# Performance work log

Measured on AMD Instinct MI355X. Metric: run time of the kernel, lower is better.

The kernel has to match this reference:

```python
import jax, jax.numpy as jnp
import numpy as np
from jax import lax

RADIUS = 0.1
K_LOCAL = 32
N_CENTROIDS = 2048


def farthest_point_sample(pos, m):
    # Greedy FPS, deterministic start at index 0 (torch version uses a random start).
    pos = lax.stop_gradient(pos)  # index selection is non-differentiable
    N = pos.shape[0]
    big = jnp.finfo(pos.dtype).max

    def step(carry, _):
        dist, current = carry
        d2 = jnp.sum((pos - pos[current]) ** 2, axis=-1)  # (N,)
        dist = jnp.minimum(dist, d2)
        nxt = jnp.argmax(dist).astype(jnp.int32)
        return (dist, nxt), current

    init = (jnp.full((N,), big, dtype=pos.dtype), jnp.int32(0))
    _, idx = lax.scan(step, init, None, length=m)
    return idx  # (m,) int32


def ball_query(pos, centers, radius, k):
    # (M, N) pairwise squared distances -- same dense form as the torch reference.
    d2 = jnp.sum((centers[:, None, :] - pos[None, :, :]) ** 2, axis=-1)
    within = d2 <= radius * radius
    big = jnp.finfo(d2.dtype).max
    masked = jnp.where(within, d2, big)
    _, idx = lax.top_k(-masked, k)              # k smallest distances
    valid = jnp.take_along_axis(within, idx, axis=1)
    fallback = jnp.broadcast_to(idx[:, :1], idx.shape)
    return jnp.where(valid, idx, fallback)      # (M, k) padded with first (nearest) idx


def setup_inputs() -> dict:
    key = jax.random.key(0)
    ks = jax.random.split(key, 5)
    N, C = 50000, 128
    scale = 1.0 / np.sqrt(C)
    return {
        "pos": jax.random.uniform(ks[0], (N, 3), dtype=jnp.float32),
        "feat_scalar": jax.random.normal(ks[1], (N, C, 1), dtype=jnp.float32),
        "feat_vector": jax.random.normal(ks[2], (N, C, 3), dtype=jnp.float32),
        "W_scalar": jax.random.normal(ks[3], (C, C), dtype=jnp.float32) * scale,
        "W_vector": jax.random.normal(ks[4], (C, C), dtype=jnp.float32) * scale,
        "b_scalar": jnp.zeros((C,), dtype=jnp.float32),
        "b_vector": jnp.zeros((C,), dtype=jnp.float32),
    }


def reference(pos, feat_scalar, feat_vector, W_scalar, W_vector, b_scalar, b_vector):
    M = min(N_CENTROIDS, pos.shape[0])
    cent_idx = farthest_point_sample(pos, M)          # (M,)
    centroids = pos[cent_idx]                         # (M, 3)
    nbr_idx = ball_query(pos, centroids, RADIUS, K_LOCAL)  # (M, k)

    def pool_mix(f, W, b):
        f_nbr = f[nbr_idx]                            # (M, k, C, d) gather
        f_pooled = jnp.max(f_nbr, axis=1)             # (M, C, d) max-pool over neighbors
        # ChannelMixer: linear mix across channel dim
        return jnp.einsum('mcd,co->mod', f_pooled, W) + b[None, :, None]

    out_scalar = pool_mix(feat_scalar, W_scalar, b_scalar)
    out_vector = pool_mix(feat_vector, W_vector, b_vector)
    return centroids, out_scalar, out_vector
```

## Files before the change

### kernel.cpp

```cpp
#include <hip/hip_runtime.h>
#include <float.h>

#define N_PTS   50000
#define M_CENT  2048
#define K_LOC   32
#define C_CH    128

typedef unsigned long long u64;
typedef unsigned int u32;

#define FPS_NB    14
#define FPS_GRID  128
#define FPS_NT    512
#define FPS_PPT   7
#define FPS_R     64
#define SLOT_U64  8
#define ROW_U64   (FPS_NB*SLOT_U64)
#define FPS_FAST_TRIPS 256
#define FPS_POLL_BOUND (1<<16)

__global__ void init_ws_kernel(u64* __restrict__ slots) {
  int t = blockIdx.x * blockDim.x + threadIdx.x;
  if (t < FPS_R * FPS_NB * SLOT_U64) slots[t] = 0ull;
}

__device__ __forceinline__ void fast_store(u64* p, u64 v) {
  asm volatile("global_store_dwordx2 %0, %1, off sc0"
               :: "v"(p), "v"(v) : "memory");
}
__device__ __forceinline__ u64 fresh_load(const u64* p) {
  u64 v;
  asm volatile("buffer_inv sc0\n\t"
               "global_load_dwordx2 %0, %1, off\n\t"
               "s_waitcnt vmcnt(0)"
               : "=v"(v) : "v"(p) : "memory");
  return v;
}
__device__ __forceinline__ u64 sc1_load(const u64* p) {
  return __hip_atomic_load(p, __ATOMIC_RELAXED, __HIP_MEMORY_SCOPE_AGENT);
}
template <bool SAFE>
__device__ __forceinline__ void slot_store(u64* p, u64 v) {
  if (SAFE) __hip_atomic_store(p, v, __ATOMIC_RELAXED, __HIP_MEMORY_SCOPE_AGENT);
  else      fast_store(p, v);
}

template <int CTRL>
__device__ __forceinline__ u32 dppmov_u(u32 v) {
  return (u32)__builtin_amdgcn_update_dpp((int)v, (int)v, CTRL, 0xf, 0xf, false);
}
template <int CTRL>
__device__ __forceinline__ float dppmov_f(float v) {
  return __int_as_float(
      __builtin_amdgcn_update_dpp(__float_as_int(v), __float_as_int(v),
                                  CTRL, 0xf, 0xf, false));
}
__device__ __forceinline__ float wave_max_f32(float v) {
  v = fmaxf(v, dppmov_f<0x111>(v));
  v = fmaxf(v, dppmov_f<0x112>(v));
  v = fmaxf(v, dppmov_f<0x114>(v));
  v = fmaxf(v, dppmov_f<0x118>(v));
  v = fmaxf(v, dppmov_f<0x142>(v));
  v = fmaxf(v, dppmov_f<0x143>(v));
  return __int_as_float(__builtin_amdgcn_readlane(__float_as_int(v), 63));
}
__device__ __forceinline__ u32 wave_max_u32(u32 v) {
  u32 t;
  t = dppmov_u<0x111>(v); v = v > t ? v : t;
  t = dppmov_u<0x112>(v); v = v > t ? v : t;
  t = dppmov_u<0x114>(v); v = v > t ? v : t;
  t = dppmov_u<0x118>(v); v = v > t ? v : t;
  t = dppmov_u<0x142>(v); v = v > t ? v : t;
  t = dppmov_u<0x143>(v); v = v > t ? v : t;
  return (u32)__builtin_amdgcn_readlane((int)v, 63);
}
__device__ __forceinline__ u32 wave_min_u32(u32 v) {
  u32 t;
  t = dppmov_u<0x111>(v); v = v < t ? v : t;
  t = dppmov_u<0x112>(v); v = v < t ? v : t;
  t = dppmov_u<0x114>(v); v = v < t ? v : t;
  t = dppmov_u<0x118>(v); v = v < t ? v : t;
  t = dppmov_u<0x142>(v); v = v < t ? v : t;
  t = dppmov_u<0x143>(v); v = v < t ? v : t;
  return (u32)__builtin_amdgcn_readlane((int)v, 63);
}

template <bool SAFE>
__device__ __forceinline__ void fps_main(
    const float* __restrict__ pos, u64* __restrict__ slots,
    float* __restrict__ cent_out, const int wid,
    uint2 (*s_w)[FPS_NT/64], float (*s_bc)[3])
{
  const int lane = threadIdx.x & 63;
  const int wv   = threadIdx.x >> 6;
  const int w    = wid * (FPS_NT/64) + wv;

  float px[FPS_PPT], py[FPS_PPT], pz[FPS_PPT], dist[FPS_PPT];
#pragma unroll
  for (int j = 0; j < FPS_PPT; j++) {
    int n = (w * FPS_PPT + j) * 64 + lane;
    if (n < N_PTS) {
      px[j] = pos[3*n+0]; py[j] = pos[3*n+1]; pz[j] = pos[3*n+2];
      dist[j] = FLT_MAX;
    } else {
      px[j] = 0.f; py[j] = 0.f; pz[j] = 0.f; dist[j] = -1.f;
    }
  }

  bool broken   = false;
  bool distrust = false;

  float cx = pos[0], cy = pos[1], cz = pos[2];

  for (int i = 0; i < M_CENT; i++) {
    if (wid == 0 && wv == 0 && lane == 0) {
      cent_out[3*i+0] = cx; cent_out[3*i+1] = cy; cent_out[3*i+2] = cz;
    }
    float lmax = -1.0f;
#pragma unroll
    for (int j = 0; j < FPS_PPT; j++) {
      int n = (w * FPS_PPT + j) * 64 + lane;
      if (n < N_PTS) {
        float dx = __fsub_rn(px[j], cx);
        float dy = __fsub_rn(py[j], cy);
        float dz = __fsub_rn(pz[j], cz);
        float d2 = __fadd_rn(__fadd_rn(__fmul_rn(dx,dx), __fmul_rn(dy,dy)),
                             __fmul_rn(dz,dz));
        float d  = fminf(dist[j], d2);
        dist[j] = d;
        lmax = fmaxf(lmax, d);
      }
    }
    float wmax = wave_max_f32(lmax);
    u32 li = 0xFFFFFFFFu;
#pragma unroll
    for (int j = 0; j < FPS_PPT; j++) {
      int n = (w * FPS_PPT + j) * 64 + lane;
      if (n < N_PTS && dist[j] == wmax) li = li < (u32)n ? li : (u32)n;
    }
    u32 widx = wave_min_u32(li);

    if (i == M_CENT - 1) break;

    if (lane == 0) s_w[i & 1][wv] = make_uint2(__float_as_uint(wmax), widx);
    __syncthreads();

    if (wv == 0) {
      uint2 kv = (lane < FPS_NT/64) ? s_w[i & 1][lane]
                                    : make_uint2(0u, 0xFFFFFFFFu);
      u32 bmaxb = wave_max_u32(kv.x);
      u32 bidx  = wave_min_u32(kv.x == bmaxb ? kv.y : 0xFFFFFFFFu);
      u64 ownkey = ((u64)bmaxb << 32) | (u64)(0xFFFFFFFFu - bidx);
      u64* row = slots + (size_t)(i & (FPS_R-1)) * ROW_U64;

      u64 got;
      if (!SAFE && broken) {
        got = (lane == wid) ? ownkey : 1ull;
      } else {
        if (lane == 0) {
          slot_store<SAFE>(&row[wid * SLOT_U64], ownkey);
          if (i >= 2)
            slot_store<SAFE>(&slots[(size_t)((i-2) & (FPS_R-1)) * ROW_U64
                                    + wid * SLOT_U64], 0ull);
        }
        got = (lane < FPS_NB) ? 0ull : 1ull;
        u64* sl = row + lane * SLOT_U64;
        if (!SAFE) {
          if (!distrust) {
            int t = 0;
            while (__ballot(got == 0ull) && t < FPS_FAST_TRIPS) {
              if (got == 0ull) got = fresh_load(sl);
              ++t;
            }
            if (__ballot(got == 0ull)) distrust = true;
          }
          int trips = 0;
          while (__ballot(got == 0ull)) {
            if (got == 0ull) got = sc1_load(sl);
            if (++trips > FPS_POLL_BOUND) {
              if (got == 0ull) got = 1ull;
              broken = true;
            }
          }
        } else {
          while (__ballot(got == 0ull)) {
            if (got == 0ull) got = sc1_load(sl);
          }
        }
      }
      u32 hi = (u32)(got >> 32), lo = (u32)got;
      u32 ic = 0xFFFFFFFFu - lo;
      if (ic >= N_PTS) ic = 0;
      float qx = 0.f, qy = 0.f, qz = 0.f;
      if (lane < FPS_NB) { qx = pos[3*ic]; qy = pos[3*ic+1]; qz = pos[3*ic+2]; }

      u32 H  = wave_max_u32(lane < FPS_NB ? hi : 0u);
      u32 LO = wave_max_u32((lane < FPS_NB && hi == H) ? lo : 0u);
      u64 msk = __ballot(lane < FPS_NB && hi == H && lo == LO);
      int L = __ffsll((long long)msk) - 1;
      float ncx = __int_as_float(__builtin_amdgcn_readlane(__float_as_int(qx), L));
      float ncy = __int_as_float(__builtin_amdgcn_readlane(__float_as_int(qy), L));
      float ncz = __int_as_float(__builtin_amdgcn_readlane(__float_as_int(qz), L));
      if (lane == 0) {
        s_bc[i & 1][0] = ncx; s_bc[i & 1][1] = ncy; s_bc[i & 1][2] = ncz;
      }
    }
    __syncthreads();
    cx = s_bc[i & 1][0]; cy = s_bc[i & 1][1]; cz = s_bc[i & 1][2];
  }
}

__global__ __launch_bounds__(FPS_NT) void fps_kernel(
    const float* __restrict__ pos,
    u64* __restrict__ slots,
    float* __restrict__ cent_out)
{
  __shared__ uint2 s_w[2][FPS_NT/64];
  __shared__ float s_bc[2][3];
  __shared__ int   s_role[2];

  if (threadIdx.x == 0) {
    u32 xcc;
    asm volatile("s_getreg_b32 %0, hwreg(HW_REG_XCC_ID, 0, 4)" : "=s"(xcc));
    xcc &= 7u;
    u64* cntp = slots + 63*ROW_U64 + (size_t)xcc * SLOT_U64 + 1;
    u64* winp = slots + 63*ROW_U64 + 8 * SLOT_U64 + 1;
    u64 t = __hip_atomic_fetch_add(cntp, 1ull, __ATOMIC_RELAXED,
                                   __HIP_MEMORY_SCOPE_AGENT);
    int ticket = (int)t;
    if (ticket == FPS_NB - 1) {
      u64 exp = 0ull;
      __hip_atomic_compare_exchange_strong(winp, &exp, (u64)(xcc + 1),
          __ATOMIC_RELAXED, __ATOMIC_RELAXED, __HIP_MEMORY_SCOPE_AGENT);
    }
    int role = -1, safe = 0;
    if (ticket < FPS_NB) {
      u64 win;
      do {
        win = __hip_atomic_load(winp, __ATOMIC_RELAXED, __HIP_MEMORY_SCOPE_AGENT);
        if (win == 0ull) __builtin_amdgcn_s_sleep(1);
      } while (win == 0ull);
      if (win == (u64)(xcc + 1)) {
        role = ticket;
        u64* hs = slots + 61*ROW_U64;
        bool okk = true;
        for (int r = 1; r <= 3 && okk; ++r) {
          fast_store(hs + (size_t)role * SLOT_U64 + 1, (u64)r);
          bool seen_all = false;
          for (int trip = 0; trip < 128 && !seen_all; ++trip) {
            int seen = 0;
            for (int j = 0; j < FPS_NB; ++j)
              seen += (fresh_load(hs + (size_t)j * SLOT_U64 + 1) >= (u64)r);
            seen_all = (seen == FPS_NB);
            if (!seen_all) __builtin_amdgcn_s_sleep(4);
          }
          okk = seen_all;
        }
        u64* okp = slots + 62*ROW_U64;
        __hip_atomic_store(okp + (size_t)role * SLOT_U64 + 1,
                           okk ? 2ull : 1ull,
                           __ATOMIC_RELAXED, __HIP_MEMORY_SCOPE_AGENT);
        for (int j = 0; j < FPS_NB; ++j) {
          u64 v;
          do {
            v = __hip_atomic_load(okp + (size_t)j * SLOT_U64 + 1,
                                  __ATOMIC_RELAXED, __HIP_MEMORY_SCOPE_AGENT);
            if (v == 0ull) __builtin_amdgcn_s_sleep(1);
          } while (v == 0ull);
          if (v == 1ull) safe = 1;
        }
      }
    }
    s_role[0] = role; s_role[1] = safe;
  }
  __syncthreads();
  const int wid = s_role[0];
  if (wid < 0) return;
  if (s_role[1]) fps_main<true >(pos, slots, cent_out, wid, s_w, s_bc);
  else           fps_main<false>(pos, slots, cent_out, wid, s_w, s_bc);
}

#define BQ_NT  256
#define BQ_CAP 2048

__global__ __launch_bounds__(BQ_NT) void ballq_kernel(
    const float* __restrict__ pos,
    const float* __restrict__ cent,
    int* __restrict__ nbr,
    int* __restrict__ nsel)
{
  __shared__ float s_d2[BQ_CAP];
  __shared__ int   s_idx[BQ_CAP];
  __shared__ int   s_count;
  __shared__ u64   s_red[BQ_NT/64];
  __shared__ u64   s_win;

  const int m = blockIdx.x, tid = threadIdx.x;
  if (tid == 0) s_count = 0;
  __syncthreads();
  const float cx = cent[3*m+0], cy = cent[3*m+1], cz = cent[3*m+2];

  for (int n = tid; n < N_PTS; n += BQ_NT) {
    float dx = __fsub_rn(cx, pos[3*n+0]);
    float dy = __fsub_rn(cy, pos[3*n+1]);
    float dz = __fsub_rn(cz, pos[3*n+2]);
    float d2 = __fadd_rn(__fadd_rn(__fmul_rn(dx,dx), __fmul_rn(dy,dy)),
                         __fmul_rn(dz,dz));
    if (d2 <= 0.01f) {
      int p = atomicAdd(&s_count, 1);
      if (p < BQ_CAP) { s_d2[p] = d2; s_idx[p] = n; }
    }
  }
  __syncthreads();
  int cnt = s_count; if (cnt > BQ_CAP) cnt = BQ_CAP;
  int ns = cnt < K_LOC ? cnt : K_LOC;

  for (int sel = 0; sel < ns; sel++) {
    u64 best = ~0ull;
    for (int p = tid; p < cnt; p += BQ_NT) {
      u64 pk = ((u64)__float_as_uint(s_d2[p]) << 32) | (u64)(u32)s_idx[p];
      if (pk < best) best = pk;
    }
#pragma unroll
    for (int off = 32; off >= 1; off >>= 1) {
      u64 o = __shfl_down(best, off, 64);
      if (o < best) best = o;
    }
    if ((tid & 63) == 0) s_red[tid >> 6] = best;
    __syncthreads();
    if (tid < 64) {
      best = (tid < BQ_NT/64) ? s_red[tid] : ~0ull;
#pragma unroll
      for (int off = 2; off >= 1; off >>= 1) {
        u64 o = __shfl_down(best, off, 64);
        if (o < best) best = o;
      }
      if (tid == 0) s_win = best;
    }
    __syncthreads();
    int widx = (int)(u32)(s_win & 0xFFFFFFFFull);
    if (tid == 0) nbr[m*K_LOC + sel] = widx;
    for (int p = tid; p < cnt; p += BQ_NT) {
      if (s_idx[p] == widx) s_d2[p] = FLT_MAX;
    }
    __syncthreads();
  }
  if (tid == 0) nsel[m] = ns;
}

__global__ __launch_bounds__(C_CH) void pool_mix_kernel(
    const float* __restrict__ fs,
    const float* __restrict__ fv,
    const float* __restrict__ Ws,
    const float* __restrict__ Wv,
    const float* __restrict__ bs,
    const float* __restrict__ bv,
    const int* __restrict__ nbr,
    const int* __restrict__ nsel,
    float* __restrict__ out_s,
    float* __restrict__ out_v)
{
  __shared__ float ps[C_CH];
  __shared__ float pv[C_CH*3];
  const int m = blockIdx.x, o = threadIdx.x;
  const int ns = nsel[m];
  float mS = -FLT_MAX, m0 = -FLT_MAX, m1 = -FLT_MAX, m2 = -FLT_MAX;
  for (int j = 0; j < ns; j++) {
    int n = nbr[m*K_LOC + j];
    mS = fmaxf(mS, fs[(size_t)n*C_CH + o]);
    const float* r = fv + (size_t)n*(C_CH*3) + 3*o;
    m0 = fmaxf(m0, r[0]); m1 = fmaxf(m1, r[1]); m2 = fmaxf(m2, r[2]);
  }
  ps[o] = mS; pv[3*o+0] = m0; pv[3*o+1] = m1; pv[3*o+2] = m2;
  __syncthreads();
  float aS = bs[o];
  float a0 = bv[o], a1 = bv[o], a2 = bv[o];
  for (int cc = 0; cc < C_CH; cc++) {
    float w1 = Ws[cc*C_CH + o];
    float w2 = Wv[cc*C_CH + o];
    aS = fmaf(ps[cc], w1, aS);
    a0 = fmaf(pv[3*cc+0], w2, a0);
    a1 = fmaf(pv[3*cc+1], w2, a1);
    a2 = fmaf(pv[3*cc+2], w2, a2);
  }
  out_s[(size_t)m*C_CH + o] = aS;
  float* ov = out_v + (size_t)m*(C_CH*3) + 3*o;
  ov[0] = a0; ov[1] = a1; ov[2] = a2;
}

extern "C" void kernel_launch(void* const* d_in, const int* in_sizes, int n_in,
                              void* d_out, int out_size, void* d_ws, size_t ws_size,
                              hipStream_t stream) {
  (void)in_sizes; (void)n_in; (void)out_size; (void)ws_size;
  const float* pos = (const float*)d_in[0];
  const float* fs  = (const float*)d_in[1];
  const float* fv  = (const float*)d_in[2];
  const float* Ws  = (const float*)d_in[3];
  const float* Wv  = (const float*)d_in[4];
  const float* bs  = (const float*)d_in[5];
  const float* bv  = (const float*)d_in[6];

  float* out      = (float*)d_out;
  float* cent_out = out;
  float* out_s    = out + 3*M_CENT;
  float* out_v    = out + 3*M_CENT + M_CENT*C_CH;

  char* ws = (char*)d_ws;
  u64* slots = (u64*)ws;
  size_t slots_bytes = (size_t)FPS_R * FPS_NB * SLOT_U64 * 8;
  int* nbr   = (int*)(ws + slots_bytes);
  int* nsel  = (int*)(ws + slots_bytes + (size_t)M_CENT*K_LOC*4);

  init_ws_kernel<<<(FPS_R*FPS_NB*SLOT_U64 + 255)/256, 256, 0, stream>>>(slots);
  fps_kernel<<<FPS_GRID, FPS_NT, 0, stream>>>(pos, slots, cent_out);
  ballq_kernel<<<M_CENT, BQ_NT, 0, stream>>>(pos, cent_out, nbr, nsel);
  pool_mix_kernel<<<M_CENT, C_CH, 0, stream>>>(fs, fv, Ws, Wv, bs, bv,
                                               nbr, nsel, out_s, out_v);
}
```

Measured before the change: 3.663 ms.

## Launch oversized FPS grid and elect one block per distinct CU per XCC

The FPS launch grows from 128 to 1024 blocks. Each block claims its hardware CU id (from HW_ID) through a CAS table, and only the first block to land on a given CU in an XCC gets a ticket. The first XCC with 14 distinct-CU blocks becomes the worker set, with a fallback election after all blocks arrive or a timeout. The aim is for the 14 cooperating FPS blocks to sit on separate CUs of one XCC, which should cut contention and speed up the spin-barrier iterations. The cost is launching many extra blocks that only poll atomics and then exit, plus a more complex election path.

```diff
diff --git a/kernel.cpp b/kernel.cpp
--- a/kernel.cpp
+++ b/kernel.cpp
@@ -10,18 +10,28 @@
 typedef unsigned int u32;
 
 #define FPS_NB    14
-#define FPS_GRID  128
+#define FPS_GRID  1024
 #define FPS_NT    512
 #define FPS_PPT   7
 #define FPS_R     64
 #define SLOT_U64  8
 #define ROW_U64   (FPS_NB*SLOT_U64)
+#define SLOTS_U64 (FPS_R*ROW_U64)
+#define CLAIM_U64 2048
+#define MISC_U64  256
+#define WS_FPS_U64 (SLOTS_U64 + CLAIM_U64 + MISC_U64)
+#define MI_CNTS(x) ((x)*8)
+#define MI_CNTR(x) ((8+(x))*8)
+#define MI_WIN     (16*8)
+#define MI_WIN2    (17*8)
+#define MI_ARR     (18*8)
 #define FPS_FAST_TRIPS 256
 #define FPS_POLL_BOUND (1<<16)
+#define STRICT_TIMEOUT 8192
 
 __global__ void init_ws_kernel(u64* __restrict__ slots) {
   int t = blockIdx.x * blockDim.x + threadIdx.x;
-  if (t < FPS_R * FPS_NB * SLOT_U64) slots[t] = 0ull;
+  if (t < WS_FPS_U64) slots[t] = 0ull;
 }
 
 __device__ __forceinline__ void fast_store(u64* p, u64 v) {
@@ -220,55 +230,99 @@
   __shared__ int   s_role[2];
 
   if (threadIdx.x == 0) {
-    u32 xcc;
+    u64* claim = slots + SLOTS_U64;
+    u64* misc  = slots + SLOTS_U64 + CLAIM_U64;
+    u32 hwid, xcc;
+    asm volatile("s_getreg_b32 %0, hwreg(HW_REG_HW_ID)" : "=s"(hwid));
     asm volatile("s_getreg_b32 %0, hwreg(HW_REG_XCC_ID, 0, 4)" : "=s"(xcc));
     xcc &= 7u;
-    u64* cntp = slots + 63*ROW_U64 + (size_t)xcc * SLOT_U64 + 1;
-    u64* winp = slots + 63*ROW_U64 + 8 * SLOT_U64 + 1;
-    u64 t = __hip_atomic_fetch_add(cntp, 1ull, __ATOMIC_RELAXED,
-                                   __HIP_MEMORY_SCOPE_AGENT);
-    int ticket = (int)t;
-    if (ticket == FPS_NB - 1) {
+    u32 cukey = (hwid >> 8) & 0xFFu;
+    int ticket = -1;
+    {
       u64 exp = 0ull;
-      __hip_atomic_compare_exchange_strong(winp, &exp, (u64)(xcc + 1),
-          __ATOMIC_RELAXED, __ATOMIC_RELAXED, __HIP_MEMORY_SCOPE_AGENT);
+      if (__hip_atomic_compare_exchange_strong(&claim[xcc*256u + cukey], &exp,
+            1ull, __ATOMIC_RELAXED, __ATOMIC_RELAXED, __HIP_MEMORY_SCOPE_AGENT)) {
+        ticket = (int)__hip_atomic_fetch_add(&misc[MI_CNTS(xcc)], 1ull,
+                     __ATOMIC_RELAXED, __HIP_MEMORY_SCOPE_AGENT);
+        if (ticket == FPS_NB - 1) {
+          u64 e = 0ull;
+          __hip_atomic_compare_exchange_strong(&misc[MI_WIN], &e, (u64)(xcc+1),
+              __ATOMIC_RELAXED, __ATOMIC_RELAXED, __HIP_MEMORY_SCOPE_AGENT);
+        }
+      }
+    }
+    __hip_atomic_fetch_add(&misc[MI_ARR], 1ull,
+                           __ATOMIC_RELAXED, __HIP_MEMORY_SCOPE_AGENT);
+    u64 win;
+    for (int trip = 0; ; ++trip) {
+      win = __hip_atomic_load(&misc[MI_WIN],
+                              __ATOMIC_RELAXED, __HIP_MEMORY_SCOPE_AGENT);
+      if (win) break;
+      u64 arr = __hip_atomic_load(&misc[MI_ARR],
+                                  __ATOMIC_RELAXED, __HIP_MEMORY_SCOPE_AGENT);
+      if (arr >= (u64)FPS_GRID || trip > STRICT_TIMEOUT) {
+        u64 mx = 0ull;
+        for (int x = 0; x < 8; ++x) {
+          u64 c = __hip_atomic_load(&misc[MI_CNTS(x)],
+                                    __ATOMIC_RELAXED, __HIP_MEMORY_SCOPE_AGENT);
+          mx = c > mx ? c : mx;
+        }
+        if (mx < (u64)FPS_NB || trip > STRICT_TIMEOUT) {
+          u64 e = 0ull;
+          __hip_atomic_compare_exchange_strong(&misc[MI_WIN], &e, 9ull,
+              __ATOMIC_RELAXED, __ATOMIC_RELAXED, __HIP_MEMORY_SCOPE_AGENT);
+        }
+      }
+      __builtin_amdgcn_s_sleep(16);
     }
     int role = -1, safe = 0;
-    if (ticket < FPS_NB) {
-      u64 win;
-      do {
-        win = __hip_atomic_load(winp, __ATOMIC_RELAXED, __HIP_MEMORY_SCOPE_AGENT);
-        if (win == 0ull) __builtin_amdgcn_s_sleep(1);
-      } while (win == 0ull);
-      if (win == (u64)(xcc + 1)) {
-        role = ticket;
-        u64* hs = slots + 61*ROW_U64;
-        bool okk = true;
-        for (int r = 1; r <= 3 && okk; ++r) {
-          fast_store(hs + (size_t)role * SLOT_U64 + 1, (u64)r);
-          bool seen_all = false;
-          for (int trip = 0; trip < 128 && !seen_all; ++trip) {
-            int seen = 0;
-            for (int j = 0; j < FPS_NB; ++j)
-              seen += (fresh_load(hs + (size_t)j * SLOT_U64 + 1) >= (u64)r);
-            seen_all = (seen == FPS_NB);
-            if (!seen_all) __builtin_amdgcn_s_sleep(4);
-          }
-          okk = seen_all;
-        }
-        u64* okp = slots + 62*ROW_U64;
-        __hip_atomic_store(okp + (size_t)role * SLOT_U64 + 1,
-                           okk ? 2ull : 1ull,
-                           __ATOMIC_RELAXED, __HIP_MEMORY_SCOPE_AGENT);
-        for (int j = 0; j < FPS_NB; ++j) {
-          u64 v;
-          do {
-            v = __hip_atomic_load(okp + (size_t)j * SLOT_U64 + 1,
-                                  __ATOMIC_RELAXED, __HIP_MEMORY_SCOPE_AGENT);
-            if (v == 0ull) __builtin_amdgcn_s_sleep(1);
-          } while (v == 0ull);
-          if (v == 1ull) safe = 1;
-        }
+    if (win <= 8ull) {
+      if (ticket >= 0 && ticket < FPS_NB && win == (u64)(xcc + 1)) role = ticket;
+    } else {
+      int t2 = (int)__hip_atomic_fetch_add(&misc[MI_CNTR(xcc)], 1ull,
+                    __ATOMIC_RELAXED, __HIP_MEMORY_SCOPE_AGENT);
+      if (t2 == FPS_NB - 1) {
+        u64 e = 0ull;
+        __hip_atomic_compare_exchange_strong(&misc[MI_WIN2], &e, (u64)(xcc+1),
+            __ATOMIC_RELAXED, __ATOMIC_RELAXED, __HIP_MEMORY_SCOPE_AGENT);
+      }
+      if (t2 < FPS_NB) {
+        u64 w2;
+        do {
+          w2 = __hip_atomic_load(&misc[MI_WIN2],
+                                 __ATOMIC_RELAXED, __HIP_MEMORY_SCOPE_AGENT);
+          if (!w2) __builtin_amdgcn_s_sleep(1);
+        } while (!w2);
+        if (w2 == (u64)(xcc + 1)) role = t2;
+      }
+    }
+    if (role >= 0) {
+      u64* hs = slots + 61*ROW_U64;
+      bool okk = true;
+      for (int r = 1; r <= 3 && okk; ++r) {
+        fast_store(hs + (size_t)role * SLOT_U64 + 1, (u64)r);
+        bool seen_all = false;
+        for (int trip = 0; trip < 128 && !seen_all; ++trip) {
+          int seen = 0;
+          for (int j = 0; j < FPS_NB; ++j)
+            seen += (fresh_load(hs + (size_t)j * SLOT_U64 + 1) >= (u64)r);
+          seen_all = (seen == FPS_NB);
+          if (!seen_all) __builtin_amdgcn_s_sleep(4);
+        }
+        okk = seen_all;
+      }
+      u64* okp = slots + 62*ROW_U64;
+      __hip_atomic_store(okp + (size_t)role * SLOT_U64 + 1,
+                         okk ? 2ull : 1ull,
+                         __ATOMIC_RELAXED, __HIP_MEMORY_SCOPE_AGENT);
+      for (int j = 0; j < FPS_NB; ++j) {
+        u64 v;
+        do {
+          v = __hip_atomic_load(okp + (size_t)j * SLOT_U64 + 1,
+                                __ATOMIC_RELAXED, __HIP_MEMORY_SCOPE_AGENT);
+          if (v == 0ull) __builtin_amdgcn_s_sleep(1);
+        } while (v == 0ull);
+        if (v == 1ull) safe = 1;
       }
     }
     s_role[0] = role; s_role[1] = safe;
@@ -407,11 +461,11 @@
 
   char* ws = (char*)d_ws;
   u64* slots = (u64*)ws;
-  size_t slots_bytes = (size_t)FPS_R * FPS_NB * SLOT_U64 * 8;
+  size_t slots_bytes = (size_t)WS_FPS_U64 * 8;
   int* nbr   = (int*)(ws + slots_bytes);
   int* nsel  = (int*)(ws + slots_bytes + (size_t)M_CENT*K_LOC*4);
 
-  init_ws_kernel<<<(FPS_R*FPS_NB*SLOT_U64 + 255)/256, 256, 0, stream>>>(slots);
+  init_ws_kernel<<<(WS_FPS_U64 + 255)/256, 256, 0, stream>>>(slots);
   fps_kernel<<<FPS_GRID, FPS_NT, 0, stream>>>(pos, slots, cent_out);
   ballq_kernel<<<M_CENT, BQ_NT, 0, stream>>>(pos, cent_out, nbr, nsel);
   pool_mix_kernel<<<M_CENT, C_CH, 0, stream>>>(fs, fv, Ws, Wv, bs, bv,
```

After: 3.761 ms. 1.03x slower.
